# Optimization experiments

Hardware: AMD Instinct MI355X
Metric: run time of the kernel (lower is better)

## Reference

```python
import jax, jax.numpy as jnp
import numpy as np

EMBED_DIM = 128
HIDDEN_DIM = 32
BN_EPS = 1e-5


def setup_inputs() -> dict:
    key = jax.random.key(0)
    ks = jax.random.split(key, 11)
    B, N, D, H = 16, 2048, EMBED_DIM, HIDDEN_DIM
    s_d = 1.0 / np.sqrt(D)
    return {
        "f_in": jax.random.normal(ks[0], (B, N, D), dtype=jnp.float32),
        "w_q": jax.random.uniform(ks[1], (H, D), jnp.float32, -s_d, s_d),
        "b_q": jax.random.uniform(ks[2], (H,), jnp.float32, -s_d, s_d),
        "w_k": jax.random.uniform(ks[3], (H, D), jnp.float32, -s_d, s_d),
        "b_k": jax.random.uniform(ks[4], (H,), jnp.float32, -s_d, s_d),
        "w_v": jax.random.uniform(ks[5], (D, D), jnp.float32, -s_d, s_d),
        "b_v": jax.random.uniform(ks[6], (D,), jnp.float32, -s_d, s_d),
        "w_l": jax.random.uniform(ks[7], (D, D), jnp.float32, -s_d, s_d),
        "b_l": jax.random.uniform(ks[8], (D,), jnp.float32, -s_d, s_d),
        "bn_gamma": jnp.ones((D,), jnp.float32),
        "bn_beta": jnp.zeros((D,), jnp.float32),
    }


def reference(f_in, w_q, b_q, w_k, b_k, w_v, b_v, w_l, b_l, bn_gamma, bn_beta):
    # Q/K/V projections: (B, N, D) -> (B, N, h) / (B, N, D)
    q = jnp.einsum("bnd,hd->bnh", f_in, w_q) + b_q
    k = jnp.einsum("bnd,hd->bnh", f_in, w_k) + b_k
    v = jnp.einsum("bnd,ed->bne", f_in, w_v) + b_v
    # scores (B, N, N); softmax over dim=1 (query axis), then L1-renorm over keys
    a = jnp.einsum("bnh,bmh->bnm", q, k)
    a = jax.nn.softmax(a, axis=1)
    a = a / jnp.sum(a, axis=2, keepdims=True)
    f_sa = jnp.einsum("bnm,bme->bne", a, v)
    # LBR: Linear -> BatchNorm (training stats over B and N) -> ReLU, residual add
    x = f_in - f_sa
    y = jnp.einsum("bnd,ed->bne", x, w_l) + b_l
    mean = jnp.mean(y, axis=(0, 1))
    var = jnp.var(y, axis=(0, 1))  # biased, as BatchNorm uses for normalization
    y = bn_gamma * (y - mean) * jax.lax.rsqrt(var + BN_EPS) + bn_beta
    return jax.nn.relu(y) + f_sa
```

## Files before the change

kernel.cpp:

```cpp
#include <hip/hip_runtime.h>
#include <stdint.h>

#define NB 16
#define NN 2048
#define ND 128
#define NH 32
#define NS (NB*NN)

typedef __attribute__((ext_vector_type(8))) short bf16x8;
typedef __attribute__((ext_vector_type(4))) float f32x4;
typedef __attribute__((ext_vector_type(16))) float f32x16;
typedef __attribute__((ext_vector_type(2))) int i32x2;

__device__ __forceinline__ unsigned short f2bf(float f){
  union { float f; unsigned int u; } v; v.f = f;
  unsigned int r = v.u + 0x7fffu + ((v.u >> 16) & 1u);
  return (unsigned short)(r >> 16);
}
__device__ __forceinline__ float bf2f(unsigned short u){
  union { unsigned int u; float f; } v; v.u = ((unsigned int)u) << 16;
  return v.f;
}
__device__ __forceinline__ float fexp2(float x){
  float r; asm("v_exp_f32 %0, %1" : "=v"(r) : "v"(x)); return r;
}
__device__ __forceinline__ void pswap(unsigned int &x, unsigned int &y){
#if __has_builtin(__builtin_amdgcn_permlane32_swap)
  i32x2 r = __builtin_amdgcn_permlane32_swap((int)x, (int)y, false, false);
  x = (unsigned int)r[0]; y = (unsigned int)r[1];
#else
  unsigned int sx = (unsigned int)__shfl_xor((int)x, 32, 64);
  unsigned int sy = (unsigned int)__shfl_xor((int)y, 32, 64);
  bool hi = ((threadIdx.x & 63) >> 5) != 0;
  unsigned int nx = hi ? sy : x;
  unsigned int ny = hi ? y  : sx;
  x = nx; y = ny;
#endif
}

__global__ __launch_bounds__(256) void k_prep(const float* wq, const float* wk, const float* wv, const float* wl,
                                              unsigned short* oq, unsigned short* ok, unsigned short* ov, unsigned short* ol){
  int i = blockIdx.x*256 + threadIdx.x;
  if (i < 4096) oq[i] = f2bf(wq[i]);
  else if (i < 8192) ok[i-4096] = f2bf(wk[i-4096]);
  else if (i < 24576) ov[i-8192] = f2bf(wv[i-8192]);
  else if (i < 40960) ol[i-24576] = f2bf(wl[i-24576]);
}

__global__ __launch_bounds__(256) void k_qkv(const float* f, const unsigned short* wbq, const unsigned short* wbk,
                                             const unsigned short* wbv, const float* bq, const float* bk, const float* bv,
                                             unsigned short* Qb, unsigned short* Kb, unsigned short* Vb){
  int tid = threadIdx.x, wave = tid>>6, lane = tid&63, lr = lane&15, lg = lane>>4;
  long r0 = (long)blockIdx.x*64 + wave*16;
  bf16x8 a[4];
  const float4* frow4 = (const float4*)(f + (r0 + lr)*ND);
  #pragma unroll
  for (int ks=0; ks<4; ks++){
    int base = ks*8 + lg*2;
    float4 x0 = frow4[base], x1 = frow4[base+1];
    bf16x8 t;
    t[0]=(short)f2bf(x0.x); t[1]=(short)f2bf(x0.y); t[2]=(short)f2bf(x0.z); t[3]=(short)f2bf(x0.w);
    t[4]=(short)f2bf(x1.x); t[5]=(short)f2bf(x1.y); t[6]=(short)f2bf(x1.z); t[7]=(short)f2bf(x1.w);
    a[ks] = t;
  }
  #pragma unroll
  for (int cs=0; cs<12; cs++){
    const unsigned short* wsrc; const float* bsrc; int cl;
    if (cs<2){ wsrc=wbq; bsrc=bq; cl=cs*16; }
    else if (cs<4){ wsrc=wbk; bsrc=bk; cl=(cs-2)*16; }
    else { wsrc=wbv; bsrc=bv; cl=(cs-4)*16; }
    f32x4 acc = {0.f,0.f,0.f,0.f};
    #pragma unroll
    for (int ks=0;ks<4;ks++){
      bf16x8 b = *(const bf16x8*)(wsrc + (cl+lr)*ND + ks*32 + lg*8);
      acc = __builtin_amdgcn_mfma_f32_16x16x32_bf16(a[ks], b, acc, 0, 0, 0);
    }
    float bias = bsrc[cl + lr];
    #pragma unroll
    for (int r=0;r<4;r++){
      float v = acc[r] + bias;
      if (cs<2) v *= 1.4426950408889634f;
      long row = r0 + lg*4 + r;
      if (cs<2) Qb[row*NH + cl+lr] = f2bf(v);
      else if (cs<4) Kb[row*NH + cl+lr] = f2bf(v);
      else Vb[row*ND + cl+lr] = f2bf(v);
    }
  }
}

__global__ __launch_bounds__(256) void k_csv(const unsigned short* Qb, const unsigned short* Kb,
                                             const unsigned short* Vb, unsigned short* VT){
  __shared__ unsigned short tr[128][65];
  __shared__ float wsh[64];
  __shared__ __align__(16) unsigned char qs[3][4096];
  int tid=threadIdx.x, wave=tid>>6, lane=tid&63, lr=lane&15, lg=lane>>4;
  int wg = (blockIdx.x & 7)*64 + (blockIdx.x >> 3);
  int b = wg >> 5;
  int m0 = (wg & 31)*64;
  const unsigned short* Qbb = Qb + (long)b*NN*NH;
  const unsigned short* Kbb = Kb + (long)b*NN*NH;
  const unsigned short* Vbb = Vb + ((long)b*NN + m0)*ND;

  auto stageQ = [&](int buf, int n0){
    int row = wave*16 + (lane>>2);
    int blk = lane & 3;
    int scol = (blk ^ ((row>>1)&3))*8;
    __builtin_amdgcn_global_load_lds(
      (const __attribute__((address_space(1))) unsigned int*)(Qbb + (long)(n0+row)*NH + scol),
      (__attribute__((address_space(3))) unsigned int*)(&qs[buf][wave*1024]), 16, 0, 0);
  };

  bf16x8 vreg[4];
  #pragma unroll
  for (int it=0; it<4; it++){
    int i = it*256 + tid;
    int r = i >> 4, c8 = (i & 15)*8;
    vreg[it] = *(const bf16x8*)(Vbb + r*ND + c8);
  }
  bf16x8 kf = *(const bf16x8*)(Kbb + (m0 + wave*16 + lr)*NH + lg*8);
  stageQ(0, 0);
  stageQ(1, 64);

  float csum = 0.f;
  int qrd = (lg ^ ((lr>>1)&3)) << 4;
  int qc = 0, qsn = 2;
  for (int it = 0; it < 32; ++it){
    if (it < 31) asm volatile("s_waitcnt vmcnt(1)" ::: "memory");
    else         asm volatile("s_waitcnt vmcnt(0)" ::: "memory");
    __builtin_amdgcn_s_barrier();
    if (it + 2 < 32) stageQ(qsn, (it+2)*64);
    asm volatile("" ::: "memory");
    #pragma unroll
    for (int u=0; u<4; u++){
      int r = u*16 + lr;
      bf16x8 qf = *(const bf16x8*)(&qs[qc][r*64 + qrd]);
      f32x4 c = {0.f,0.f,0.f,0.f};
      c = __builtin_amdgcn_mfma_f32_16x16x32_bf16(qf, kf, c, 0, 0, 0);
      csum += fexp2(c[0]) + fexp2(c[1]) + fexp2(c[2]) + fexp2(c[3]);
    }
    qc = (qc==2)?0:qc+1;
    qsn = (qsn==2)?0:qsn+1;
  }
  csum += __shfl_xor(csum, 16, 64);
  csum += __shfl_xor(csum, 32, 64);
  #pragma unroll
  for (int it=0; it<4; it++){
    int i = it*256 + tid;
    int r = i >> 4, c8 = (i & 15)*8;
    #pragma unroll
    for (int j=0;j<8;j++) tr[c8+j][r] = (unsigned short)vreg[it][j];
  }
  if (lg == 0) wsh[wave*16 + lr] = 1.f / csum;
  __syncthreads();
  unsigned short* VTb = VT + (long)b*160*NN;
  #pragma unroll
  for (int it=0; it<9; it++){
    int i = it*256 + tid;
    int e = i >> 4, m4 = (i & 15)*4;
    ushort4 o;
    if (e < 128){
      o.x = f2bf(bf2f(tr[e][m4+0]) * wsh[m4+0]);
      o.y = f2bf(bf2f(tr[e][m4+1]) * wsh[m4+1]);
      o.z = f2bf(bf2f(tr[e][m4+2]) * wsh[m4+2]);
      o.w = f2bf(bf2f(tr[e][m4+3]) * wsh[m4+3]);
    } else if (e == 128){
      o.x = f2bf(wsh[m4+0]); o.y = f2bf(wsh[m4+1]);
      o.z = f2bf(wsh[m4+2]); o.w = f2bf(wsh[m4+3]);
    } else { o.x = o.y = o.z = o.w = 0; }
    *(ushort4*)(VTb + (long)e*NN + m0 + m4) = o;
  }
  {
    int e = 144 + (tid >> 4), m4 = (tid & 15)*4;
    ushort4 z; z.x = z.y = z.z = z.w = 0;
    *(ushort4*)(VTb + (long)e*NN + m0 + m4) = z;
  }
}

__global__ __launch_bounds__(256) void k_pv(const unsigned short* Qb, const unsigned short* Kb,
                                            const unsigned short* VT, unsigned short* pnum, float* pden){
  __shared__ __align__(16) unsigned char vts[3][20480];
  int tid=threadIdx.x, wave=tid>>6, lane=tid&63;
  int l31 = lane & 31, H = lane >> 5;
  int wg = (blockIdx.x & 7)*64 + (blockIdx.x >> 3);
  int half = wg & 1;
  int bq = wg >> 1;
  int b = bq >> 4;
  int q0 = (bq & 15)*128 + wave*32;
  int mbase = half*1024;
  const int NT2 = 16;
  const unsigned short* Qbb = Qb + (long)b*NN*NH;
  const unsigned short* Kbb = Kb + (long)b*NN*NH;
  const unsigned short* VTb = VT + (long)b*160*NN;

  auto stageV = [&](int buf, int m0c){
    #pragma unroll
    for (int t=0;t<5;t++){
      int i = wave*5 + t;
      int e = i*8 + (lane>>3);
      int sblk = (lane&7) ^ (e&7);
      __builtin_amdgcn_global_load_lds(
        (const __attribute__((address_space(1))) unsigned int*)(VTb + (long)e*NN + m0c + sblk*8),
        (__attribute__((address_space(3))) unsigned int*)(&vts[buf][i*1024]), 16, 0, 0);
    }
  };

  bf16x8 qf0 = *(const bf16x8*)(Qbb + (long)(q0 + l31)*NH + 8*H);
  bf16x8 qf1 = *(const bf16x8*)(Qbb + (long)(q0 + l31)*NH + 16 + 8*H);

  f32x16 acc[5];
  #pragma unroll
  for (int c=0;c<5;c++)
    #pragma unroll
    for (int r=0;r<16;r++) acc[c][r] = 0.f;

  union U { unsigned int u[4]; bf16x8 v; };

  auto SCORE = [&](bf16x8 a0, bf16x8 a1, bf16x8 b0, bf16x8 b1, unsigned int* w){
    #pragma unroll
    for (int t=0;t<2;t++){
      f32x16 s;
      #pragma unroll
      for (int r=0;r<16;r++) s[r] = 0.f;
      s = __builtin_amdgcn_mfma_f32_32x32x16_bf16(t ? b0 : a0, qf0, s, 0, 0, 0);
      s = __builtin_amdgcn_mfma_f32_32x32x16_bf16(t ? b1 : a1, qf1, s, 0, 0, 0);
      #pragma unroll
      for (int r=0;r<16;r++) s[r] = fexp2(s[r]);
      unsigned int pk[8];
      #pragma unroll
      for (int p=0;p<8;p++)
        asm("v_cvt_pk_bf16_f32 %0, %1, %2" : "=v"(pk[p]) : "v"(s[2*p]), "v"(s[2*p+1]));
      pswap(pk[0], pk[2]);
      pswap(pk[1], pk[3]);
      pswap(pk[4], pk[6]);
      pswap(pk[5], pk[7]);
      #pragma unroll
      for (int j=0;j<8;j++) w[t*8+j] = pk[j];
    }
  };

  auto PV = [&](const unsigned int* w, const unsigned char* vcur){
    __builtin_amdgcn_s_setprio(1);
    #pragma unroll
    for (int t=0;t<2;t++){
      #pragma unroll
      for (int ksl=0; ksl<2; ksl++){
        int KS = 2*t + ksl;
        U fa;
        #pragma unroll
        for (int i2=0;i2<4;i2++) fa.u[i2] = w[t*8 + ksl*4 + i2];
        #pragma unroll
        for (int c=0;c<5;c++){
          int e = c*32 + l31;
          bf16x8 vb = *(const bf16x8*)(vcur + (e<<7) + (((2*KS + H) ^ (e&7))<<4));
          acc[c] = __builtin_amdgcn_mfma_f32_32x32x16_bf16(fa.v, vb, acc[c], 0, 0, 0);
        }
      }
    }
    __builtin_amdgcn_s_setprio(0);
  };

  stageV(0, mbase);
  stageV(1, mbase + 64);
  asm volatile("" ::: "memory");
  bf16x8 k00 = *(const bf16x8*)(Kbb + (long)(mbase + l31)*NH + 8*H);
  bf16x8 k01 = *(const bf16x8*)(Kbb + (long)(mbase + l31)*NH + 16 + 8*H);
  bf16x8 k10 = *(const bf16x8*)(Kbb + (long)(mbase + 32 + l31)*NH + 8*H);
  bf16x8 k11 = *(const bf16x8*)(Kbb + (long)(mbase + 32 + l31)*NH + 16 + 8*H);
  asm volatile("s_waitcnt vmcnt(0)" ::: "memory");
  unsigned int eA[16], eB[16];
  SCORE(k00, k01, k10, k11, eA);

  int vc = 0, vs = 2;
  auto BODY = [&](int it, unsigned int* Ein, unsigned int* Eout){
    __builtin_amdgcn_s_barrier();
    asm volatile("" ::: "memory");
    bool pf = (it + 1 < NT2);
    bf16x8 n00, n01, n10, n11;
    if (pf){
      long mb = mbase + (long)(it+1)*64;
      n00 = *(const bf16x8*)(Kbb + (mb + l31)*NH + 8*H);
      n01 = *(const bf16x8*)(Kbb + (mb + l31)*NH + 16 + 8*H);
      n10 = *(const bf16x8*)(Kbb + (mb + 32 + l31)*NH + 8*H);
      n11 = *(const bf16x8*)(Kbb + (mb + 32 + l31)*NH + 16 + 8*H);
    }
    asm volatile("" ::: "memory");
    if (it + 2 < NT2) stageV(vs, mbase + (it+2)*64);
    asm volatile("" ::: "memory");
    PV(Ein, &vts[vc][0]);
    if (pf){
      if (it + 2 < NT2) asm volatile("s_waitcnt vmcnt(5)" ::: "memory");
      else              asm volatile("s_waitcnt vmcnt(0)" ::: "memory");
      __builtin_amdgcn_sched_barrier(0);
      SCORE(n00, n01, n10, n11, Eout);
    }
    vc = (vc==2)?0:vc+1;
    vs = (vs==2)?0:vs+1;
  };

  for (int it2 = 0; it2 < NT2; it2 += 2){
    BODY(it2,   eA, eB);
    BODY(it2+1, eB, eA);
  }

  unsigned short* pn = pnum + (long)half*NS*ND + (long)b*NN*ND;
  float* pd = pden + (long)half*NS + (long)b*NN;
  #pragma unroll
  for (int r=0;r<16;r++){
    int rho = (r&3) + 8*(r>>2) + 4*H;
    long q = q0 + rho;
    #pragma unroll
    for (int c=0;c<4;c++)
      pn[q*ND + c*32 + l31] = f2bf(acc[c][r]);
    if (l31 == 0) pd[q] = acc[4][r];
  }
}

__global__ __launch_bounds__(256) void k_lin(const float* f, const unsigned short* pnum, const float* pden,
                                             const unsigned short* wbl, const float* bl,
                                             unsigned short* fsab, unsigned short* ybuf, float* part){
  __shared__ float psum[4][128], psq[4][128];
  int tid=threadIdx.x, wave=tid>>6, lane=tid&63, lr=lane&15, lg=lane>>4;
  long r0 = (long)blockIdx.x*64 + wave*16;
  long row = r0 + lr;
  float rinv = 1.f / (pden[row] + pden[NS + row]);
  bf16x8 a[4];
  {
    const float4* fr4 = (const float4*)(f + row*ND);
    const unsigned short* p0 = pnum + row*ND;
    const unsigned short* p1 = pnum + (long)NS*ND + row*ND;
    #pragma unroll
    for (int ks=0;ks<4;ks++){
      int c8 = ks*4 + lg;
      float4 x0 = fr4[c8*2], x1 = fr4[c8*2+1];
      bf16x8 v0 = *(const bf16x8*)(p0 + c8*8);
      bf16x8 v1 = *(const bf16x8*)(p1 + c8*8);
      float xf[8] = {x0.x,x0.y,x0.z,x0.w,x1.x,x1.y,x1.z,x1.w};
      bf16x8 t, fs;
      #pragma unroll
      for (int j=0;j<8;j++){
        float sa = (bf2f((unsigned short)v0[j]) + bf2f((unsigned short)v1[j])) * rinv;
        fs[j] = (short)f2bf(sa);
        t[j] = (short)f2bf(xf[j] - bf2f((unsigned short)fs[j]));
      }
      a[ks] = t;
      *(bf16x8*)(fsab + row*ND + c8*8) = fs;
    }
  }
  #pragma unroll
  for (int cs=0;cs<8;cs++){
    f32x4 acc = {0.f,0.f,0.f,0.f};
    #pragma unroll
    for (int ks=0;ks<4;ks++){
      bf16x8 bfr = *(const bf16x8*)(wbl + (cs*16+lr)*ND + ks*32 + lg*8);
      acc = __builtin_amdgcn_mfma_f32_16x16x32_bf16(a[ks], bfr, acc, 0, 0, 0);
    }
    float bias = bl[cs*16+lr];
    float l1=0.f, l2=0.f;
    #pragma unroll
    for (int r=0;r<4;r++){
      float y = acc[r] + bias;
      ybuf[(r0 + lg*4 + r)*ND + cs*16 + lr] = f2bf(y);
      l1 += y; l2 += y*y;
    }
    l1 += __shfl_xor(l1,16,64); l1 += __shfl_xor(l1,32,64);
    l2 += __shfl_xor(l2,16,64); l2 += __shfl_xor(l2,32,64);
    if (lg==0){ psum[wave][cs*16+lr] = l1; psq[wave][cs*16+lr] = l2; }
  }
  __syncthreads();
  if (tid < 128){
    float t1 = psum[0][tid]+psum[1][tid]+psum[2][tid]+psum[3][tid];
    float t2 = psq[0][tid]+psq[1][tid]+psq[2][tid]+psq[3][tid];
    part[tid*512 + blockIdx.x] = t1;
    part[65536 + tid*512 + blockIdx.x] = t2;
  }
}

__global__ __launch_bounds__(64) void k_bnred(const float* part, const float* gamma, const float* beta, float* bnstat){
  int c = blockIdx.x, t = threadIdx.x;
  float s=0.f, q=0.f;
  for (int i=t; i<512; i+=64){ s += part[c*512+i]; q += part[65536 + c*512+i]; }
  #pragma unroll
  for (int m=1; m<64; m<<=1){ s += __shfl_xor(s,m,64); q += __shfl_xor(q,m,64); }
  if (t==0){
    float mean = s * (1.f/(float)NS);
    float var  = q * (1.f/(float)NS) - mean*mean;
    float rstd = rsqrtf(var + 1e-5f);
    float sc = gamma[c]*rstd;
    bnstat[c] = sc;
    bnstat[128+c] = beta[c] - mean*sc;
  }
}

__global__ __launch_bounds__(256) void k_final(const unsigned short* ybuf, const unsigned short* fsab, const float* bnstat,
                                               float* out){
  long i0 = ((long)blockIdx.x*256 + threadIdx.x)*8;
  int c0 = (int)(i0 & (ND-1));
  bf16x8 yv = *(const bf16x8*)(ybuf + i0);
  bf16x8 fv = *(const bf16x8*)(fsab + i0);
  f32x4 o0, o1;
  #pragma unroll
  for (int j=0;j<8;j++){
    int c = c0 + j;
    float v = bf2f((unsigned short)yv[j]) * bnstat[c] + bnstat[128+c];
    v = v > 0.f ? v : 0.f;
    float r = v + bf2f((unsigned short)fv[j]);
    if (j<4) o0[j] = r; else o1[j-4] = r;
  }
  *(f32x4*)(out + i0) = o0;
  *(f32x4*)(out + i0 + 4) = o1;
}

extern "C" void kernel_launch(void* const* d_in, const int* in_sizes, int n_in,
                              void* d_out, int out_size, void* d_ws, size_t ws_size,
                              hipStream_t stream){
  const float* f_in  = (const float*)d_in[0];
  const float* w_q   = (const float*)d_in[1];
  const float* b_q   = (const float*)d_in[2];
  const float* w_k   = (const float*)d_in[3];
  const float* b_k   = (const float*)d_in[4];
  const float* w_v   = (const float*)d_in[5];
  const float* b_v   = (const float*)d_in[6];
  const float* w_l   = (const float*)d_in[7];
  const float* b_l   = (const float*)d_in[8];
  const float* gamma = (const float*)d_in[9];
  const float* beta  = (const float*)d_in[10];
  float* out = (float*)d_out;
  char* ws = (char*)d_ws;

  unsigned short* wbq = (unsigned short*)(ws + 0);
  unsigned short* wbk = (unsigned short*)(ws + 8192);
  unsigned short* wbv = (unsigned short*)(ws + 16384);
  unsigned short* wbl = (unsigned short*)(ws + 49152);
  unsigned short* Qb  = (unsigned short*)(ws + 81920);
  float*          part= (float*)(ws + 81920);
  unsigned short* Kb  = (unsigned short*)(ws + 2179072);
  unsigned short* VT  = (unsigned short*)(ws + 4276224);
  unsigned short* ybuf= (unsigned short*)(ws + 4276224);
  unsigned short* Vb  = (unsigned short*)(ws + 14761984);
  unsigned short* fsab= (unsigned short*)(ws + 14761984);
  unsigned short* pnum= (unsigned short*)(ws + 23150592);
  float*          pden= (float*)(ws + 39927808);
  float*          bnst= (float*)(ws + 40189952);

  k_prep  <<<160, 256, 0, stream>>>(w_q, w_k, w_v, w_l, wbq, wbk, wbv, wbl);
  k_qkv   <<<512, 256, 0, stream>>>(f_in, wbq, wbk, wbv, b_q, b_k, b_v, Qb, Kb, Vb);
  k_csv   <<<512, 256, 0, stream>>>(Qb, Kb, Vb, VT);
  k_pv    <<<512, 256, 0, stream>>>(Qb, Kb, VT, pnum, pden);
  k_lin   <<<512, 256, 0, stream>>>(f_in, pnum, pden, wbl, b_l, fsab, ybuf, part);
  k_bnred <<<128, 64, 0, stream>>>(part, gamma, beta, bnst);
  k_final <<<2048,256, 0, stream>>>(ybuf, fsab, bnst, out);
}
```

Measured before the change: 109.9 us.

## Split PV key range into quarters and simplify to double-buffered loop

The attention PV kernel now splits each query block's key range four ways instead of two, launching 1024 workgroups. Each one processes 8 key tiles. The software pipeline is simplified from triple-buffered V staging with score computation a step ahead to a double-buffered loop that computes scores and PV in the same iteration. The linear kernel now sums four partial numerators and denominators. This aims for more parallelism and lower LDS use per block, at the cost of twice the partial-result traffic and a less overlapped inner loop.

```diff
diff --git a/kernel.cpp b/kernel.cpp
--- a/kernel.cpp
+++ b/kernel.cpp
@@ -177,17 +177,18 @@
 }
 
 __global__ __launch_bounds__(256) void k_pv(const unsigned short* Qb, const unsigned short* Kb,
-                                            const unsigned short* VT, unsigned short* pnum, float* pden){
-  __shared__ __align__(16) unsigned char vts[3][20480];
+                                            const unsigned short* VT,
+                                            unsigned short* pnum, float* pden){
+  __shared__ __align__(16) unsigned char vts[2][20480];
   int tid=threadIdx.x, wave=tid>>6, lane=tid&63;
   int l31 = lane & 31, H = lane >> 5;
-  int wg = (blockIdx.x & 7)*64 + (blockIdx.x >> 3);
-  int half = wg & 1;
-  int bq = wg >> 1;
+  int wg = (blockIdx.x & 7)*128 + (blockIdx.x >> 3);
+  int quarter = wg & 3;
+  int bq = wg >> 2;
   int b = bq >> 4;
   int q0 = (bq & 15)*128 + wave*32;
-  int mbase = half*1024;
-  const int NT2 = 16;
+  int mbase = quarter*512;
+  const int NT = 8;
   const unsigned short* Qbb = Qb + (long)b*NN*NH;
   const unsigned short* Kbb = Kb + (long)b*NN*NH;
   const unsigned short* VTb = VT + (long)b*160*NN;
@@ -206,6 +207,9 @@
 
   bf16x8 qf0 = *(const bf16x8*)(Qbb + (long)(q0 + l31)*NH + 8*H);
   bf16x8 qf1 = *(const bf16x8*)(Qbb + (long)(q0 + l31)*NH + 16 + 8*H);
+  asm volatile("" ::: "memory");
+  stageV(0, mbase);
+  asm volatile("" ::: "memory");
 
   f32x16 acc[5];
   #pragma unroll
@@ -215,14 +219,29 @@
 
   union U { unsigned int u[4]; bf16x8 v; };
 
-  auto SCORE = [&](bf16x8 a0, bf16x8 a1, bf16x8 b0, bf16x8 b1, unsigned int* w){
+  int cur = 0;
+  for (int it = 0; it < NT; ++it){
+    __builtin_amdgcn_s_barrier();
+    long mb = mbase + (long)it*64;
+    bf16x8 k00 = *(const bf16x8*)(Kbb + (mb + l31)*NH + 8*H);
+    bf16x8 k01 = *(const bf16x8*)(Kbb + (mb + l31)*NH + 16 + 8*H);
+    bf16x8 k10 = *(const bf16x8*)(Kbb + (mb + 32 + l31)*NH + 8*H);
+    bf16x8 k11 = *(const bf16x8*)(Kbb + (mb + 32 + l31)*NH + 16 + 8*H);
+    asm volatile("" ::: "memory");
+    if (it + 1 < NT) stageV(cur^1, mbase + (it+1)*64);
+    asm volatile("" ::: "memory");
+    if (it + 1 < NT) asm volatile("s_waitcnt vmcnt(5)" ::: "memory");
+    else             asm volatile("s_waitcnt vmcnt(0)" ::: "memory");
+    __builtin_amdgcn_sched_barrier(0);
+    const unsigned char* vcur = &vts[cur][0];
+
     #pragma unroll
     for (int t=0;t<2;t++){
       f32x16 s;
       #pragma unroll
       for (int r=0;r<16;r++) s[r] = 0.f;
-      s = __builtin_amdgcn_mfma_f32_32x32x16_bf16(t ? b0 : a0, qf0, s, 0, 0, 0);
-      s = __builtin_amdgcn_mfma_f32_32x32x16_bf16(t ? b1 : a1, qf1, s, 0, 0, 0);
+      s = __builtin_amdgcn_mfma_f32_32x32x16_bf16(t ? k10 : k00, qf0, s, 0, 0, 0);
+      s = __builtin_amdgcn_mfma_f32_32x32x16_bf16(t ? k11 : k01, qf1, s, 0, 0, 0);
       #pragma unroll
       for (int r=0;r<16;r++) s[r] = fexp2(s[r]);
       unsigned int pk[8];
@@ -233,21 +252,13 @@
       pswap(pk[1], pk[3]);
       pswap(pk[4], pk[6]);
       pswap(pk[5], pk[7]);
-      #pragma unroll
-      for (int j=0;j<8;j++) w[t*8+j] = pk[j];
-    }
-  };
-
-  auto PV = [&](const unsigned int* w, const unsigned char* vcur){
-    __builtin_amdgcn_s_setprio(1);
-    #pragma unroll
-    for (int t=0;t<2;t++){
+      __builtin_amdgcn_s_setprio(1);
       #pragma unroll
       for (int ksl=0; ksl<2; ksl++){
         int KS = 2*t + ksl;
         U fa;
         #pragma unroll
-        for (int i2=0;i2<4;i2++) fa.u[i2] = w[t*8 + ksl*4 + i2];
+        for (int i2=0;i2<4;i2++) fa.u[i2] = pk[ksl*4 + i2];
         #pragma unroll
         for (int c=0;c<5;c++){
           int e = c*32 + l31;
@@ -255,55 +266,12 @@
           acc[c] = __builtin_amdgcn_mfma_f32_32x32x16_bf16(fa.v, vb, acc[c], 0, 0, 0);
         }
       }
-    }
-    __builtin_amdgcn_s_setprio(0);
-  };
-
-  stageV(0, mbase);
-  stageV(1, mbase + 64);
-  asm volatile("" ::: "memory");
-  bf16x8 k00 = *(const bf16x8*)(Kbb + (long)(mbase + l31)*NH + 8*H);
-  bf16x8 k01 = *(const bf16x8*)(Kbb + (long)(mbase + l31)*NH + 16 + 8*H);
-  bf16x8 k10 = *(const bf16x8*)(Kbb + (long)(mbase + 32 + l31)*NH + 8*H);
-  bf16x8 k11 = *(const bf16x8*)(Kbb + (long)(mbase + 32 + l31)*NH + 16 + 8*H);
-  asm volatile("s_waitcnt vmcnt(0)" ::: "memory");
-  unsigned int eA[16], eB[16];
-  SCORE(k00, k01, k10, k11, eA);
-
-  int vc = 0, vs = 2;
-  auto BODY = [&](int it, unsigned int* Ein, unsigned int* Eout){
-    __builtin_amdgcn_s_barrier();
-    asm volatile("" ::: "memory");
-    bool pf = (it + 1 < NT2);
-    bf16x8 n00, n01, n10, n11;
-    if (pf){
-      long mb = mbase + (long)(it+1)*64;
-      n00 = *(const bf16x8*)(Kbb + (mb + l31)*NH + 8*H);
-      n01 = *(const bf16x8*)(Kbb + (mb + l31)*NH + 16 + 8*H);
-      n10 = *(const bf16x8*)(Kbb + (mb + 32 + l31)*NH + 8*H);
-      n11 = *(const bf16x8*)(Kbb + (mb + 32 + l31)*NH + 16 + 8*H);
-    }
-    asm volatile("" ::: "memory");
-    if (it + 2 < NT2) stageV(vs, mbase + (it+2)*64);
-    asm volatile("" ::: "memory");
-    PV(Ein, &vts[vc][0]);
-    if (pf){
-      if (it + 2 < NT2) asm volatile("s_waitcnt vmcnt(5)" ::: "memory");
-      else              asm volatile("s_waitcnt vmcnt(0)" ::: "memory");
-      __builtin_amdgcn_sched_barrier(0);
-      SCORE(n00, n01, n10, n11, Eout);
-    }
-    vc = (vc==2)?0:vc+1;
-    vs = (vs==2)?0:vs+1;
-  };
-
-  for (int it2 = 0; it2 < NT2; it2 += 2){
-    BODY(it2,   eA, eB);
-    BODY(it2+1, eB, eA);
-  }
-
-  unsigned short* pn = pnum + (long)half*NS*ND + (long)b*NN*ND;
-  float* pd = pden + (long)half*NS + (long)b*NN;
+      __builtin_amdgcn_s_setprio(0);
+    }
+    cur ^= 1;
+  }
+  unsigned short* pn = pnum + (long)quarter*NS*ND + (long)b*NN*ND;
+  float* pd = pden + (long)quarter*NS + (long)b*NN;
   #pragma unroll
   for (int r=0;r<16;r++){
     int rho = (r&3) + 8*(r>>2) + 4*H;
@@ -322,23 +290,28 @@
   int tid=threadIdx.x, wave=tid>>6, lane=tid&63, lr=lane&15, lg=lane>>4;
   long r0 = (long)blockIdx.x*64 + wave*16;
   long row = r0 + lr;
-  float rinv = 1.f / (pden[row] + pden[NS + row]);
+  float rinv = 1.f / (pden[row] + pden[NS + row] + pden[2L*NS + row] + pden[3L*NS + row]);
   bf16x8 a[4];
   {
     const float4* fr4 = (const float4*)(f + row*ND);
     const unsigned short* p0 = pnum + row*ND;
     const unsigned short* p1 = pnum + (long)NS*ND + row*ND;
+    const unsigned short* p2 = pnum + 2L*NS*ND + row*ND;
+    const unsigned short* p3 = pnum + 3L*NS*ND + row*ND;
     #pragma unroll
     for (int ks=0;ks<4;ks++){
       int c8 = ks*4 + lg;
       float4 x0 = fr4[c8*2], x1 = fr4[c8*2+1];
       bf16x8 v0 = *(const bf16x8*)(p0 + c8*8);
       bf16x8 v1 = *(const bf16x8*)(p1 + c8*8);
+      bf16x8 v2 = *(const bf16x8*)(p2 + c8*8);
+      bf16x8 v3 = *(const bf16x8*)(p3 + c8*8);
       float xf[8] = {x0.x,x0.y,x0.z,x0.w,x1.x,x1.y,x1.z,x1.w};
       bf16x8 t, fs;
       #pragma unroll
       for (int j=0;j<8;j++){
-        float sa = (bf2f((unsigned short)v0[j]) + bf2f((unsigned short)v1[j])) * rinv;
+        float sa = (bf2f((unsigned short)v0[j]) + bf2f((unsigned short)v1[j])
+                  + bf2f((unsigned short)v2[j]) + bf2f((unsigned short)v3[j])) * rinv;
         fs[j] = (short)f2bf(sa);
         t[j] = (short)f2bf(xf[j] - bf2f((unsigned short)fs[j]));
       }
@@ -439,13 +412,13 @@
   unsigned short* Vb  = (unsigned short*)(ws + 14761984);
   unsigned short* fsab= (unsigned short*)(ws + 14761984);
   unsigned short* pnum= (unsigned short*)(ws + 23150592);
-  float*          pden= (float*)(ws + 39927808);
-  float*          bnst= (float*)(ws + 40189952);
+  float*          pden= (float*)(ws + 56705024);
+  float*          bnst= (float*)(ws + 57229312);
 
   k_prep  <<<160, 256, 0, stream>>>(w_q, w_k, w_v, w_l, wbq, wbk, wbv, wbl);
   k_qkv   <<<512, 256, 0, stream>>>(f_in, wbq, wbk, wbv, b_q, b_k, b_v, Qb, Kb, Vb);
   k_csv   <<<512, 256, 0, stream>>>(Qb, Kb, Vb, VT);
-  k_pv    <<<512, 256, 0, stream>>>(Qb, Kb, VT, pnum, pden);
+  k_pv    <<<1024,256, 0, stream>>>(Qb, Kb, VT, pnum, pden);
   k_lin   <<<512, 256, 0, stream>>>(f_in, pnum, pden, wbl, b_l, fsab, ybuf, part);
   k_bnred <<<128, 64, 0, stream>>>(part, gamma, beta, bnst);
   k_final <<<2048,256, 0, stream>>>(ybuf, fsab, bnst, out);
```

Result: no change. 111.9 us (+1.8%).
